# Performance work log

Measured on AMD Instinct MI355X. Metric: run time of the kernel, lower is better.

## Reference

```python
import jax, jax.numpy as jnp
import numpy as np

NUM_HEADS = 16
KEY_SIZE = 64
MODEL = NUM_HEADS * KEY_SIZE
B, S = 4, 2048
NEG = jnp.float32(-1e9)


def alibi_bidirectional_bias(num_heads, seq_len):
    # slopes for num_heads//2 heads: 1 / x**(i+1), x = 24**(1/h)
    h = num_heads // 2
    x = 24.0 ** (1.0 / h)
    slopes = (1.0 / x ** jnp.arange(1, h + 1, dtype=jnp.float32))[:, None, None]  # [h,1,1]
    i = jnp.arange(seq_len)
    rel = (i[None, :] - i[:, None]).astype(jnp.float32)  # rel[i,j] = j - i
    # forward (causal): tril(j - i) + (-1e9 strictly above diag)
    fwd = slopes * jnp.tril(rel) + jnp.triu(jnp.full((seq_len, seq_len), NEG), k=1)
    # backward (anti-causal): triu(i - j) + (-1e9 strictly below diag)
    bwd = slopes * jnp.triu(-rel) + jnp.tril(jnp.full((seq_len, seq_len), NEG), k=-1)
    return jnp.concatenate([fwd, bwd], axis=0)  # [num_heads, S, S]


def setup_inputs() -> dict:
    key = jax.random.key(0)
    ks = jax.random.split(key, 11)
    sc = 0.02
    d = {
        "query": jax.random.normal(ks[0], (B, S, MODEL), jnp.float32),
        "key": jax.random.normal(ks[1], (B, S, MODEL), jnp.float32),
        "value": jax.random.normal(ks[2], (B, S, MODEL), jnp.float32),
        "Wq": jax.random.normal(ks[3], (MODEL, MODEL), jnp.float32) * sc,
        "bq": jnp.zeros((MODEL,), jnp.float32),
        "Wk": jax.random.normal(ks[4], (MODEL, MODEL), jnp.float32) * sc,
        "bk": jnp.zeros((MODEL,), jnp.float32),
        "Wv": jax.random.normal(ks[5], (MODEL, MODEL), jnp.float32) * sc,
        "bv": jnp.zeros((MODEL,), jnp.float32),
        "Wo": jax.random.normal(ks[6], (MODEL, MODEL), jnp.float32) * sc,
        "bo": jnp.zeros((MODEL,), jnp.float32),
    }
    return d


def reference(query, key, value, Wq, bq, Wk, bk, Wv, bv, Wo, bo):
    b, s, _ = query.shape
    H, D = NUM_HEADS, KEY_SIZE

    def proj(x, W, bias):
        return (x @ W.T + bias).reshape(b, s, H, D).transpose(0, 2, 1, 3)  # [B,H,S,D]

    q = proj(query, Wq, bq)
    k = proj(key, Wk, bk)
    v = proj(value, Wv, bv)

    bias = alibi_bidirectional_bias(H, s)  # [H,S,S], broadcasts over batch
    scores = jnp.einsum("bhqd,bhkd->bhqk", q, k) / jnp.sqrt(jnp.float32(D)) + bias
    attn = jax.nn.softmax(scores, axis=-1)
    out = jnp.einsum("bhqk,bhkd->bhqd", attn, v)
    out = out.transpose(0, 2, 1, 3).reshape(b, s, H * D)
    return out @ Wo.T + bo
```

## Files before the change

### kernel.cpp

```cpp
#include <hip/hip_runtime.h>
#include <hip/hip_bf16.h>
#include <stdint.h>

typedef unsigned short u16;
typedef __attribute__((ext_vector_type(8))) __bf16 bf16x8;
typedef __attribute__((ext_vector_type(4))) float f32x4;
typedef __attribute__((ext_vector_type(4))) unsigned int u32x4;

#define S_LEN 2048
#define NHEAD 16
#define HDIM 64
#define DMODEL 1024
#define NBATCH 4
#define MTOK (NBATCH * S_LEN)

__device__ __forceinline__ u16 f2bf(float f) {
    uint32_t u = __float_as_uint(f);
    u += 0x7fffu + ((u >> 16) & 1u);
    return (u16)(u >> 16);
}

__device__ __forceinline__ void gld_lds16(const u16* g, u16* l) {
    __builtin_amdgcn_global_load_lds(
        (const __attribute__((address_space(1))) void*)g,
        (__attribute__((address_space(3))) void*)l, 16, 0, 0);
}

__global__ __launch_bounds__(256) void cast_all(
        const float* __restrict__ q, const float* __restrict__ k, const float* __restrict__ v,
        const float* __restrict__ wq, const float* __restrict__ wk,
        const float* __restrict__ wv, const float* __restrict__ wo,
        u16* __restrict__ xq, u16* __restrict__ xk, u16* __restrict__ xv,
        u16* __restrict__ wqb, u16* __restrict__ wkb, u16* __restrict__ wvb,
        u16* __restrict__ wob) {
    size_t idx4 = (size_t)blockIdx.x * 256 + threadIdx.x;
    const float* src;
    u16* dst;
    size_t off;
    if (idx4 < (size_t)3 << 21) {
        int t = (int)(idx4 >> 21);
        off = (idx4 & ((1u << 21) - 1)) * 4;
        src = (t == 0) ? q : (t == 1) ? k : v;
        dst = (t == 0) ? xq : (t == 1) ? xk : xv;
    } else {
        size_t w = idx4 - ((size_t)3 << 21);
        int t = (int)(w >> 18);
        off = (w & ((1u << 18) - 1)) * 4;
        src = (t == 0) ? wq : (t == 1) ? wk : (t == 2) ? wv : wo;
        dst = (t == 0) ? wqb : (t == 1) ? wkb : (t == 2) ? wvb : wob;
    }
    float4 val = *(const float4*)(src + off);
    ushort4 o;
    o.x = f2bf(val.x); o.y = f2bf(val.y); o.z = f2bf(val.z); o.w = f2bf(val.w);
    *(ushort4*)(dst + off) = o;
}

#define TM 128
#define TN 128
#define BK 64

__device__ __forceinline__ void gemm_body(const u16* __restrict__ A,
                                          const u16* __restrict__ W,
                                          const float* __restrict__ bias,
                                          void* __restrict__ outp, int mode,
                                          int m0, int n0) {
    __shared__ __align__(16) u16 As[TM * BK];
    __shared__ __align__(16) u16 Bs[TN * BK];
    const int tid  = threadIdx.x;
    const int lane = tid & 63;
    const int wv   = tid >> 6;
    const int l16  = lane & 15;
    const int quad = lane >> 4;
    const int wm   = (wv >> 1) * 64;
    const int wn   = (wv & 1) * 64;

    f32x4 acc[4][4];
#pragma unroll
    for (int i = 0; i < 4; i++)
#pragma unroll
        for (int j = 0; j < 4; j++) acc[i][j] = {};

    const int sr  = lane >> 3;
    const int sc7 = (lane & 7) ^ sr;
    const u16* gA = A + (size_t)(m0 + wv * 32 + sr) * DMODEL + sc7 * 8;
    const u16* gB = W + (size_t)(n0 + wv * 32 + sr) * DMODEL + sc7 * 8;
    u16* lA = As + wv * 32 * BK;
    u16* lB = Bs + wv * 32 * BK;

    const int cA = quad ^ (l16 & 7);
    const int cB = (quad + 4) ^ (l16 & 7);

    for (int kb = 0; kb < DMODEL; kb += BK) {
#pragma unroll
        for (int g = 0; g < 4; g++)
            gld_lds16(gA + kb + (size_t)(g * 8) * DMODEL, lA + g * 8 * BK);
#pragma unroll
        for (int g = 0; g < 4; g++)
            gld_lds16(gB + kb + (size_t)(g * 8) * DMODEL, lB + g * 8 * BK);
        __builtin_amdgcn_s_waitcnt(0x0F70);
        __syncthreads();

        bf16x8 af0[4], af1[4], bf0[4], bf1[4];
#pragma unroll
        for (int i = 0; i < 4; i++) {
            const u16* ap = &As[(wm + i * 16 + l16) * BK];
            af0[i] = *(const bf16x8*)(ap + cA * 8);
            af1[i] = *(const bf16x8*)(ap + cB * 8);
        }
#pragma unroll
        for (int j = 0; j < 4; j++) {
            const u16* bp = &Bs[(wn + j * 16 + l16) * BK];
            bf0[j] = *(const bf16x8*)(bp + cA * 8);
            bf1[j] = *(const bf16x8*)(bp + cB * 8);
        }
#pragma unroll
        for (int i = 0; i < 4; i++)
#pragma unroll
            for (int j = 0; j < 4; j++)
                acc[i][j] = __builtin_amdgcn_mfma_f32_16x16x32_bf16(af0[i], bf0[j], acc[i][j], 0, 0, 0);
#pragma unroll
        for (int i = 0; i < 4; i++)
#pragma unroll
            for (int j = 0; j < 4; j++)
                acc[i][j] = __builtin_amdgcn_mfma_f32_16x16x32_bf16(af1[i], bf1[j], acc[i][j], 0, 0, 0);
        __syncthreads();
    }

#pragma unroll
    for (int j = 0; j < 4; j++) {
        int n = n0 + wn + j * 16 + l16;
        float bv = bias[n];
#pragma unroll
        for (int i = 0; i < 4; i++) {
            int mbase = m0 + wm + i * 16 + quad * 4;
#pragma unroll
            for (int r = 0; r < 4; r++) {
                int m = mbase + r;
                float v = acc[i][j][r] + bv;
                if (mode == 2) {
                    ((float*)outp)[(size_t)m * DMODEL + n] = v;
                } else {
                    int b = m >> 11, s = m & (S_LEN - 1);
                    int h = n >> 6, d = n & 63;
                    u16* o = (u16*)outp;
                    size_t idx = (mode == 0)
                        ? ((((size_t)(b * NHEAD + h)) * S_LEN + s) * HDIM + d)
                        : ((((size_t)(b * NHEAD + h)) * HDIM + d) * S_LEN + s);
                    o[idx] = f2bf(v);
                }
            }
        }
    }
}

__device__ __forceinline__ void gemm_coords(int& m0, int& n0) {
    const int lid = blockIdx.x + 8 * blockIdx.y;
    const int xcd = lid & 7;
    const int s   = lid >> 3;
    n0 = (s & 7) * TN;
    m0 = ((s >> 3) + 8 * xcd) * TM;
}

__global__ __launch_bounds__(256) void gemm_qkv(
        const u16* __restrict__ xq, const u16* __restrict__ xk, const u16* __restrict__ xv,
        const u16* __restrict__ wq, const u16* __restrict__ wk, const u16* __restrict__ wv,
        const float* __restrict__ bq, const float* __restrict__ bk, const float* __restrict__ bv,
        u16* __restrict__ Qb, u16* __restrict__ Kb, u16* __restrict__ Vb) {
    int z = blockIdx.z;
    const u16* A   = (z == 0) ? xq : (z == 1) ? xk : xv;
    const u16* W   = (z == 0) ? wq : (z == 1) ? wk : wv;
    const float* b = (z == 0) ? bq : (z == 1) ? bk : bv;
    u16* out       = (z == 0) ? Qb : (z == 1) ? Kb : Vb;
    int m0, n0;
    gemm_coords(m0, n0);
    gemm_body(A, W, b, out, (z == 2) ? 1 : 0, m0, n0);
}

__global__ __launch_bounds__(256) void gemm_one(
        const u16* __restrict__ A, const u16* __restrict__ W,
        const float* __restrict__ bias, void* __restrict__ out, int mode) {
    int m0, n0;
    gemm_coords(m0, n0);
    gemm_body(A, W, bias, out, mode, m0, n0);
}

__global__ __launch_bounds__(256, 4) void flash_kernel(
        const u16* __restrict__ Q, const u16* __restrict__ K,
        const u16* __restrict__ Vt, u16* __restrict__ AO) {
    __shared__ __align__(16) u16 Ksm[2][64 * 64];
    __shared__ __align__(16) u16 Vsm[2][64 * 64];
    __shared__ __align__(16) u16 Psm[4][16 * 64];

    const int tid  = threadIdx.x;
    const int wv   = tid >> 6;
    const int lane = tid & 63;
    const int l16  = lane & 15;
    const int quad = lane >> 4;

    const int lid   = blockIdx.x + 16 * blockIdx.y;
    const int xcd   = lid & 7;
    const int slot  = lid >> 3;
    const int bh    = xcd + 8 * (slot >> 4);
    const int g_idx = slot & 15;

    const int h    = bh & (NHEAD - 1);
    const int b    = bh >> 4;
    const bool fwd = (h < 8);
    const int sgn  = fwd ? 1 : -1;
    const float slope2 = __builtin_amdgcn_exp2f(-(float)((h & 7) + 1) * 0.5731203125901445f)
                         * 1.4426950408889634f;
    const float cL = 0.18033688011112042f;

    const u16* Kg = K + (size_t)bh * S_LEN * HDIM;
    const u16* Vg = Vt + (size_t)bh * HDIM * S_LEN;

    const int sr = lane >> 3;
    const int sc = (lane & 7) ^ sr;
    const int r0 = 16 * wv;

    const int cA = quad ^ (l16 & 7);
    const int cB = (quad + 4) ^ (l16 & 7);

    float brt[4][4];
#pragma unroll
    for (int t = 0; t < 4; t++)
#pragma unroll
        for (int r = 0; r < 4; r++)
            brt[t][r] = slope2 * (float)(sgn * (16 * t + l16 - (quad * 4 + r))) - 16.0f;

    int poff[4][4];
#pragma unroll
    for (int r = 0; r < 4; r++) {
        const int prow = quad * 4 + r;
        const int pr7  = prow & 7;
#pragma unroll
        for (int t = 0; t < 4; t++)
            poff[r][t] = prow * 64 + (((2 * t + (l16 >> 3)) ^ pr7) * 8) + (l16 & 7);
    }

    bf16x8 ones;
#pragma unroll
    for (int j = 0; j < 8; j++) ones[j] = (__bf16)1.0f;

    const float dkq = slope2 * (float)(sgn * 64);

#pragma unroll 1
    for (int half = 0; half < 2; half++) {
        const int g  = half ? (31 - g_idx) : g_idx;
        const int q0 = g * 64 + wv * 16;
        const u16* Qp = Q + ((size_t)bh * S_LEN + q0) * HDIM;
        const bf16x8 aq0 = *(const bf16x8*)(Qp + l16 * HDIM + quad * 8);
        const bf16x8 aq1 = *(const bf16x8*)(Qp + l16 * HDIM + 32 + quad * 8);

        f32x4 o[4], osum = {};
#pragma unroll
        for (int dt = 0; dt < 4; dt++) o[dt] = {};

        const int kt0 = fwd ? 0 : g;
        const int kt1 = fwd ? g : (S_LEN / 64 - 1);

        __syncthreads();
        const u16* kg = Kg + ((size_t)(kt0 * 64) + r0 + sr) * 64 + sc * 8;
        const u16* vg = Vg + (size_t)(r0 + sr) * S_LEN + kt0 * 64 + sc * 8;
        gld_lds16(kg,              &Ksm[0][r0 * 64]);
        gld_lds16(kg + 8 * 64,     &Ksm[0][(r0 + 8) * 64]);
        gld_lds16(vg,              &Vsm[0][r0 * 64]);
        gld_lds16(vg + 8 * S_LEN,  &Vsm[0][(r0 + 8) * 64]);
        kg += 64 * 64;
        vg += 64;

        float kq = slope2 * (float)(sgn * (kt0 * 64 - q0));

        int buf = 0;
        for (int kt = kt0; kt <= kt1; ++kt) {
            __builtin_amdgcn_s_waitcnt(0x0F70);
            __syncthreads();
            if (kt < kt1) {
                gld_lds16(kg,             &Ksm[buf ^ 1][r0 * 64]);
                gld_lds16(kg + 8 * 64,    &Ksm[buf ^ 1][(r0 + 8) * 64]);
                gld_lds16(vg,             &Vsm[buf ^ 1][r0 * 64]);
                gld_lds16(vg + 8 * S_LEN, &Vsm[buf ^ 1][(r0 + 8) * 64]);
                kg += 64 * 64;
                vg += 64;
            }
            const u16* Ks = &Ksm[buf][0];
            const u16* Vs = &Vsm[buf][0];

            f32x4 st[4];
#pragma unroll
            for (int t = 0; t < 4; t++) {
                const u16* kp = Ks + (16 * t + l16) * 64;
                bf16x8 k0 = *(const bf16x8*)(kp + cA * 8);
                bf16x8 k1 = *(const bf16x8*)(kp + cB * 8);
                f32x4 c = {};
                c = __builtin_amdgcn_mfma_f32_16x16x32_bf16(aq0, k0, c, 0, 0, 0);
                c = __builtin_amdgcn_mfma_f32_16x16x32_bf16(aq1, k1, c, 0, 0, 0);
                st[t] = c;
            }

            float p[4][4];
            if (kt == g) {
#pragma unroll
                for (int r = 0; r < 4; r++) {
                    const int qg = q0 + quad * 4 + r;
#pragma unroll
                    for (int t = 0; t < 4; t++) {
                        const int kg2 = kt * 64 + 16 * t + l16;
                        const bool ok = fwd ? (kg2 <= qg) : (kg2 >= qg);
                        float s2 = fmaf(st[t][r], cL, brt[t][r] + kq);
                        p[t][r] = ok ? __builtin_amdgcn_exp2f(s2) : 0.0f;
                    }
                }
            } else {
#pragma unroll
                for (int r = 0; r < 4; r++)
#pragma unroll
                    for (int t = 0; t < 4; t++)
                        p[t][r] = __builtin_amdgcn_exp2f(fmaf(st[t][r], cL, brt[t][r] + kq));
            }
            kq += dkq;

            u16* Pw = &Psm[wv][0];
#pragma unroll
            for (int r = 0; r < 4; r++)
#pragma unroll
                for (int t = 0; t < 4; t++)
                    Pw[poff[r][t]] = f2bf(p[t][r]);
            __builtin_amdgcn_s_waitcnt(0xC07F);
            bf16x8 pf0 = *(const bf16x8*)(&Pw[l16 * 64 + cA * 8]);
            bf16x8 pf1 = *(const bf16x8*)(&Pw[l16 * 64 + cB * 8]);

#pragma unroll
            for (int dt = 0; dt < 4; dt++) {
                const u16* vp = Vs + (dt * 16 + l16) * 64;
                bf16x8 v0 = *(const bf16x8*)(vp + cA * 8);
                bf16x8 v1 = *(const bf16x8*)(vp + cB * 8);
                o[dt] = __builtin_amdgcn_mfma_f32_16x16x32_bf16(pf0, v0, o[dt], 0, 0, 0);
                o[dt] = __builtin_amdgcn_mfma_f32_16x16x32_bf16(pf1, v1, o[dt], 0, 0, 0);
            }
            osum = __builtin_amdgcn_mfma_f32_16x16x32_bf16(pf0, ones, osum, 0, 0, 0);
            osum = __builtin_amdgcn_mfma_f32_16x16x32_bf16(pf1, ones, osum, 0, 0, 0);
            buf ^= 1;
        }

#pragma unroll
        for (int r = 0; r < 4; r++) {
            float inv = 1.0f / osum[r];
            int qg = q0 + quad * 4 + r;
            u16* op = AO + ((size_t)b * S_LEN + qg) * DMODEL + h * HDIM;
#pragma unroll
            for (int dt = 0; dt < 4; dt++)
                op[dt * 16 + l16] = f2bf(o[dt][r] * inv);
        }
    }
}

extern "C" void kernel_launch(void* const* d_in, const int* in_sizes, int n_in,
                              void* d_out, int out_size, void* d_ws, size_t ws_size,
                              hipStream_t stream) {
    const float* query = (const float*)d_in[0];
    const float* key   = (const float*)d_in[1];
    const float* value = (const float*)d_in[2];
    const float* Wq    = (const float*)d_in[3];
    const float* bq    = (const float*)d_in[4];
    const float* Wk    = (const float*)d_in[5];
    const float* bk    = (const float*)d_in[6];
    const float* Wv    = (const float*)d_in[7];
    const float* bv    = (const float*)d_in[8];
    const float* Wo    = (const float*)d_in[9];
    const float* bo    = (const float*)d_in[10];

    const size_t Xe = (size_t)MTOK * DMODEL;
    const size_t We = (size_t)DMODEL * DMODEL;
    u16* xq  = (u16*)d_ws;
    u16* xk  = xq + Xe;
    u16* xv  = xk + Xe;
    u16* wqb = xv + Xe;
    u16* wkb = wqb + We;
    u16* wvb = wkb + We;
    u16* wob = wvb + We;
    u16* Qb  = wob + We;
    u16* Kb  = Qb + Xe;
    u16* Vb  = Kb + Xe;
    u16* AO  = Vb + Xe;

    cast_all<<<dim3(28672), dim3(256), 0, stream>>>(
        query, key, value, Wq, Wk, Wv, Wo,
        xq, xk, xv, wqb, wkb, wvb, wob);

    gemm_qkv<<<dim3(DMODEL / TN, MTOK / TM, 3), dim3(256), 0, stream>>>(
        xq, xk, xv, wqb, wkb, wvb, bq, bk, bv, Qb, Kb, Vb);

    flash_kernel<<<dim3(16, NBATCH * NHEAD), dim3(256), 0, stream>>>(Qb, Kb, Vb, AO);

    gemm_one<<<dim3(DMODEL / TN, MTOK / TM, 1), dim3(256), 0, stream>>>(AO, wob, bo, d_out, 2);
}
```

Before: 329.6 us.

## Rewrite projection GEMMs as 256x256 tiles with double-buffered async LDS pipeline

The projection GEMMs move from 128x128 tiles with 256 threads and a single-buffered load/sync/compute loop to 256x256 tiles with 512 threads (8 waves). LDS is double-buffered and split into four quadrant phases that interleave global-to-LDS loads with MFMA work, using explicit barriers, waitcnt and setprio. This raises per-block data reuse and overlaps memory latency with compute, at the cost of more LDS per block, more registers, and fewer blocks (128 per GEMM), which may leave parts of the device idle.

```diff
diff --git a/kernel.cpp b/kernel.cpp
--- a/kernel.cpp
+++ b/kernel.cpp
@@ -5,7 +5,6 @@
 typedef unsigned short u16;
 typedef __attribute__((ext_vector_type(8))) __bf16 bf16x8;
 typedef __attribute__((ext_vector_type(4))) float f32x4;
-typedef __attribute__((ext_vector_type(4))) unsigned int u32x4;
 
 #define S_LEN 2048
 #define NHEAD 16
@@ -55,93 +54,137 @@
     *(ushort4*)(dst + off) = o;
 }
 
-#define TM 128
-#define TN 128
-#define BK 64
-
-__device__ __forceinline__ void gemm_body(const u16* __restrict__ A,
-                                          const u16* __restrict__ W,
-                                          const float* __restrict__ bias,
-                                          void* __restrict__ outp, int mode,
-                                          int m0, int n0) {
-    __shared__ __align__(16) u16 As[TM * BK];
-    __shared__ __align__(16) u16 Bs[TN * BK];
+#define KTILES (DMODEL / 64)
+
+#define STAGE_A(buf, g, kt) do { \
+    gld_lds16(gA0 + (size_t)(g) * 64 * DMODEL + (kt) * 64, &Asm[buf][g][cb0 * 64]); \
+    gld_lds16(gA1 + (size_t)(g) * 64 * DMODEL + (kt) * 64, &Asm[buf][g][cb1 * 64]); \
+} while (0)
+
+#define STAGE_B(buf, g, kt) do { \
+    gld_lds16(gB0 + (size_t)(g) * 32 * DMODEL + (kt) * 64, &Bsm[buf][g][cb0 * 64]); \
+    gld_lds16(gB1 + (size_t)(g) * 32 * DMODEL + (kt) * 64, &Bsm[buf][g][cb1 * 64]); \
+} while (0)
+
+#define READ_A(buf, qm) do { \
+    _Pragma("unroll") \
+    for (int f = 0; f < 4; ++f) { \
+        const u16* ap = &Asm[buf][qm][(wm * 64 + f * 16 + l16) * 64]; \
+        af[f][0] = *(const bf16x8*)(ap + cA * 8); \
+        af[f][1] = *(const bf16x8*)(ap + cB * 8); \
+    } \
+} while (0)
+
+#define READ_B(buf, qn) do { \
+    _Pragma("unroll") \
+    for (int j = 0; j < 2; ++j) { \
+        const u16* bp = &Bsm[buf][qn][(wn * 32 + j * 16 + l16) * 64]; \
+        bfr[(qn) * 2 + j][0] = *(const bf16x8*)(bp + cA * 8); \
+        bfr[(qn) * 2 + j][1] = *(const bf16x8*)(bp + cB * 8); \
+    } \
+} while (0)
+
+#define PH_TAIL(qm, qn) do { \
+    __builtin_amdgcn_s_barrier(); \
+    __builtin_amdgcn_s_waitcnt(0xC07F);       \
+    __builtin_amdgcn_sched_barrier(0); \
+    __builtin_amdgcn_s_setprio(1); \
+    _Pragma("unroll") \
+    for (int f = 0; f < 4; ++f) \
+        _Pragma("unroll") \
+        for (int j = 0; j < 2; ++j) { \
+            acc[(qm) * 4 + f][(qn) * 2 + j] = __builtin_amdgcn_mfma_f32_16x16x32_bf16( \
+                af[f][0], bfr[(qn) * 2 + j][0], acc[(qm) * 4 + f][(qn) * 2 + j], 0, 0, 0); \
+            acc[(qm) * 4 + f][(qn) * 2 + j] = __builtin_amdgcn_mfma_f32_16x16x32_bf16( \
+                af[f][1], bfr[(qn) * 2 + j][1], acc[(qm) * 4 + f][(qn) * 2 + j], 0, 0, 0); \
+        } \
+    __builtin_amdgcn_s_setprio(0); \
+    __builtin_amdgcn_s_barrier(); \
+} while (0)
+
+__device__ __forceinline__ void gemm_body256(const u16* __restrict__ A,
+                                             const u16* __restrict__ W,
+                                             const float* __restrict__ bias,
+                                             void* __restrict__ outp, int mode,
+                                             int m0, int n0) {
+    __shared__ __align__(16) u16 Asm[2][2][128 * 64];
+    __shared__ __align__(16) u16 Bsm[2][2][128 * 64];
+
     const int tid  = threadIdx.x;
     const int lane = tid & 63;
     const int wv   = tid >> 6;
+    const int wm   = wv >> 2;
+    const int wn   = wv & 3;
     const int l16  = lane & 15;
     const int quad = lane >> 4;
-    const int wm   = (wv >> 1) * 64;
-    const int wn   = (wv & 1) * 64;
-
-    f32x4 acc[4][4];
-#pragma unroll
-    for (int i = 0; i < 4; i++)
-#pragma unroll
-        for (int j = 0; j < 4; j++) acc[i][j] = {};
-
-    const int sr  = lane >> 3;
-    const int sc7 = (lane & 7) ^ sr;
-    const u16* gA = A + (size_t)(m0 + wv * 32 + sr) * DMODEL + sc7 * 8;
-    const u16* gB = W + (size_t)(n0 + wv * 32 + sr) * DMODEL + sc7 * 8;
-    u16* lA = As + wv * 32 * BK;
-    u16* lB = Bs + wv * 32 * BK;
 
     const int cA = quad ^ (l16 & 7);
     const int cB = (quad + 4) ^ (l16 & 7);
 
-    for (int kb = 0; kb < DMODEL; kb += BK) {
-#pragma unroll
-        for (int g = 0; g < 4; g++)
-            gld_lds16(gA + kb + (size_t)(g * 8) * DMODEL, lA + g * 8 * BK);
-#pragma unroll
-        for (int g = 0; g < 4; g++)
-            gld_lds16(gB + kb + (size_t)(g * 8) * DMODEL, lB + g * 8 * BK);
-        __builtin_amdgcn_s_waitcnt(0x0F70);
-        __syncthreads();
-
-        bf16x8 af0[4], af1[4], bf0[4], bf1[4];
-#pragma unroll
-        for (int i = 0; i < 4; i++) {
-            const u16* ap = &As[(wm + i * 16 + l16) * BK];
-            af0[i] = *(const bf16x8*)(ap + cA * 8);
-            af1[i] = *(const bf16x8*)(ap + cB * 8);
-        }
-#pragma unroll
-        for (int j = 0; j < 4; j++) {
-            const u16* bp = &Bs[(wn + j * 16 + l16) * BK];
-            bf0[j] = *(const bf16x8*)(bp + cA * 8);
-            bf1[j] = *(const bf16x8*)(bp + cB * 8);
-        }
-#pragma unroll
-        for (int i = 0; i < 4; i++)
-#pragma unroll
-            for (int j = 0; j < 4; j++)
-                acc[i][j] = __builtin_amdgcn_mfma_f32_16x16x32_bf16(af0[i], bf0[j], acc[i][j], 0, 0, 0);
-#pragma unroll
-        for (int i = 0; i < 4; i++)
-#pragma unroll
-            for (int j = 0; j < 4; j++)
-                acc[i][j] = __builtin_amdgcn_mfma_f32_16x16x32_bf16(af1[i], bf1[j], acc[i][j], 0, 0, 0);
-        __syncthreads();
+    const int sr = lane >> 3;
+    const int sc = (lane & 7) ^ sr;
+    const int cb0 = wv * 16;
+    const int cb1 = wv * 16 + 8;
+    const u16* gA0 = A + (size_t)(m0 + (cb0 >> 6) * 128 + (cb0 & 63) + sr) * DMODEL + sc * 8;
+    const u16* gA1 = A + (size_t)(m0 + (cb1 >> 6) * 128 + (cb1 & 63) + sr) * DMODEL + sc * 8;
+    const u16* gB0 = W + (size_t)(n0 + (cb0 >> 5) * 64 + (cb0 & 31) + sr) * DMODEL + sc * 8;
+    const u16* gB1 = W + (size_t)(n0 + (cb1 >> 5) * 64 + (cb1 & 31) + sr) * DMODEL + sc * 8;
+
+    f32x4 acc[8][4];
+#pragma unroll
+    for (int i = 0; i < 8; ++i)
+#pragma unroll
+        for (int j = 0; j < 4; ++j) acc[i][j] = {};
+
+    bf16x8 af[4][2];
+    bf16x8 bfr[4][2];
+
+    STAGE_A(0, 0, 0);
+    STAGE_B(0, 0, 0);
+    STAGE_B(0, 1, 0);
+    STAGE_A(0, 1, 0);
+    STAGE_A(1, 0, 1);
+    STAGE_B(1, 0, 1);
+    __builtin_amdgcn_s_waitcnt(0x0F74);
+    __builtin_amdgcn_s_barrier();
+
+#pragma unroll 1
+    for (int i = 0; i < KTILES / 2 - 1; ++i) {
+        const int t1 = 2 * i + 1, t2 = 2 * i + 2, t3 = 2 * i + 3;
+        READ_A(0, 0); READ_B(0, 0); STAGE_A(1, 1, t1);            PH_TAIL(0, 0);
+        READ_B(0, 1);               STAGE_B(1, 1, t1);            PH_TAIL(0, 1);
+        READ_A(0, 1);               STAGE_A(0, 0, t2);            PH_TAIL(1, 0);
+        STAGE_B(0, 0, t2); __builtin_amdgcn_s_waitcnt(0x0F74);    PH_TAIL(1, 1);
+        READ_A(1, 0); READ_B(1, 0); STAGE_B(0, 1, t2);            PH_TAIL(0, 0);
+        READ_B(1, 1);               STAGE_A(0, 1, t2);            PH_TAIL(0, 1);
+        READ_A(1, 1);               STAGE_A(1, 0, t3);            PH_TAIL(1, 0);
+        STAGE_B(1, 0, t3); __builtin_amdgcn_s_waitcnt(0x0F74);    PH_TAIL(1, 1);
     }
-
-#pragma unroll
-    for (int j = 0; j < 4; j++) {
-        int n = n0 + wn + j * 16 + l16;
-        float bv = bias[n];
-#pragma unroll
-        for (int i = 0; i < 4; i++) {
-            int mbase = m0 + wm + i * 16 + quad * 4;
-#pragma unroll
-            for (int r = 0; r < 4; r++) {
-                int m = mbase + r;
-                float v = acc[i][j][r] + bv;
+    READ_A(0, 0); READ_B(0, 0); STAGE_A(1, 1, KTILES - 1);        PH_TAIL(0, 0);
+    READ_B(0, 1);               STAGE_B(1, 1, KTILES - 1);        PH_TAIL(0, 1);
+    READ_A(0, 1);                                                 PH_TAIL(1, 0);
+    __builtin_amdgcn_s_waitcnt(0x0F70);             PH_TAIL(1, 1);
+    READ_A(1, 0); READ_B(1, 0);                                   PH_TAIL(0, 0);
+    READ_B(1, 1);                                                 PH_TAIL(0, 1);
+    READ_A(1, 1);                                                 PH_TAIL(1, 0);
+                                                                  PH_TAIL(1, 1);
+
+#pragma unroll
+    for (int fn = 0; fn < 4; ++fn) {
+        const int n = n0 + wn * 64 + (fn >> 1) * 32 + (fn & 1) * 16 + l16;
+        const float bvl = bias[n];
+#pragma unroll
+        for (int fm = 0; fm < 8; ++fm) {
+            const int mb = m0 + wm * 128 + (fm >> 2) * 64 + (fm & 3) * 16 + quad * 4;
+#pragma unroll
+            for (int r = 0; r < 4; ++r) {
+                const int m = mb + r;
+                const float v = acc[fm][fn][r] + bvl;
                 if (mode == 2) {
                     ((float*)outp)[(size_t)m * DMODEL + n] = v;
                 } else {
-                    int b = m >> 11, s = m & (S_LEN - 1);
-                    int h = n >> 6, d = n & 63;
+                    const int b = m >> 11, s = m & (S_LEN - 1);
+                    const int h = n >> 6, d = n & 63;
                     u16* o = (u16*)outp;
                     size_t idx = (mode == 0)
                         ? ((((size_t)(b * NHEAD + h)) * S_LEN + s) * HDIM + d)
@@ -153,15 +196,21 @@
     }
 }
 
-__device__ __forceinline__ void gemm_coords(int& m0, int& n0) {
-    const int lid = blockIdx.x + 8 * blockIdx.y;
+#undef STAGE_A
+#undef STAGE_B
+#undef READ_A
+#undef READ_B
+#undef PH_TAIL
+
+__device__ __forceinline__ void gemm_coords256(int& m0, int& n0) {
+    const int lid = blockIdx.x;
     const int xcd = lid & 7;
     const int s   = lid >> 3;
-    n0 = (s & 7) * TN;
-    m0 = ((s >> 3) + 8 * xcd) * TM;
-}
-
-__global__ __launch_bounds__(256) void gemm_qkv(
+    n0 = (s & 3) * 256;
+    m0 = (4 * xcd + (s >> 2)) * 256;
+}
+
+__global__ __launch_bounds__(512, 2) void gemm_qkv(
         const u16* __restrict__ xq, const u16* __restrict__ xk, const u16* __restrict__ xv,
         const u16* __restrict__ wq, const u16* __restrict__ wk, const u16* __restrict__ wv,
         const float* __restrict__ bq, const float* __restrict__ bk, const float* __restrict__ bv,
@@ -172,16 +221,16 @@
     const float* b = (z == 0) ? bq : (z == 1) ? bk : bv;
     u16* out       = (z == 0) ? Qb : (z == 1) ? Kb : Vb;
     int m0, n0;
-    gemm_coords(m0, n0);
-    gemm_body(A, W, b, out, (z == 2) ? 1 : 0, m0, n0);
-}
-
-__global__ __launch_bounds__(256) void gemm_one(
+    gemm_coords256(m0, n0);
+    gemm_body256(A, W, b, out, (z == 2) ? 1 : 0, m0, n0);
+}
+
+__global__ __launch_bounds__(512, 2) void gemm_one(
         const u16* __restrict__ A, const u16* __restrict__ W,
         const float* __restrict__ bias, void* __restrict__ out, int mode) {
     int m0, n0;
-    gemm_coords(m0, n0);
-    gemm_body(A, W, bias, out, mode, m0, n0);
+    gemm_coords256(m0, n0);
+    gemm_body256(A, W, bias, out, mode, m0, n0);
 }
 
 __global__ __launch_bounds__(256, 4) void flash_kernel(
@@ -388,10 +437,10 @@
         query, key, value, Wq, Wk, Wv, Wo,
         xq, xk, xv, wqb, wkb, wvb, wob);
 
-    gemm_qkv<<<dim3(DMODEL / TN, MTOK / TM, 3), dim3(256), 0, stream>>>(
+    gemm_qkv<<<dim3(128, 1, 3), dim3(512), 0, stream>>>(
         xq, xk, xv, wqb, wkb, wvb, bq, bk, bv, Qb, Kb, Vb);
 
     flash_kernel<<<dim3(16, NBATCH * NHEAD), dim3(256), 0, stream>>>(Qb, Kb, Vb, AO);
 
-    gemm_one<<<dim3(DMODEL / TN, MTOK / TM, 1), dim3(256), 0, stream>>>(AO, wob, bo, d_out, 2);
-}
+    gemm_one<<<dim3(128), dim3(512), 0, stream>>>(AO, wob, bo, d_out, 2);
+}
```

New measurement: 368.5 us. 1.12x slower.
